# Performance work log

Measured on AMD Instinct MI355X. Metric: run time of the kernel, lower is better.

The kernel has to match this reference:

```python
import jax, jax.numpy as jnp
import numpy as np
from jax import lax

# --- config (matches init_kwargs) ---
D = 1024        # hidden_dim
H = 16          # num_heads
DH = D // H     # head dim
S = 5           # num_saccades
W = 128         # window_size
BK = 32         # block_size
TAU = 1.0       # gumbel temperature
DFF = 4 * D
EPS = 1e-5


def _ln(x, g, b):
    m = jnp.mean(x, axis=-1, keepdims=True)
    v = jnp.mean(jnp.square(x - m), axis=-1, keepdims=True)
    return (x - m) * lax.rsqrt(v + EPS) * g + b


def setup_inputs() -> dict:
    key = jax.random.key(0)
    ks = jax.random.split(key, 16)
    B, L = 4, 2048
    NB = L // BK
    sd = 0.02
    inp = {
        "hidden_states": jax.random.normal(ks[0], (B, L, D), jnp.float32),
        "gumbel_u": jax.random.uniform(ks[1], (S, B, NB), jnp.float32),
        "ln1_g": jnp.ones((D,), jnp.float32),
        "ln1_b": jnp.zeros((D,), jnp.float32),
        "ln2_g": jnp.ones((D,), jnp.float32),
        "ln2_b": jnp.zeros((D,), jnp.float32),
        "w_sal": jax.random.normal(ks[2], (D,), jnp.float32) * sd,
        "b_sal": jnp.zeros((), jnp.float32),
        "in_proj_w": jax.random.normal(ks[3], (3 * D, D), jnp.float32) * sd,
        "in_proj_b": jnp.zeros((3 * D,), jnp.float32),
        "out_proj_w": jax.random.normal(ks[4], (D, D), jnp.float32) * sd,
        "out_proj_b": jnp.zeros((D,), jnp.float32),
        "w_fc": jax.random.normal(ks[5], (D, DFF), jnp.float32) * sd,
        "b_fc": jnp.zeros((DFF,), jnp.float32),
        "w_proj": jax.random.normal(ks[6], (DFF, D), jnp.float32) * sd,
        "b_proj": jnp.zeros((D,), jnp.float32),
    }
    return inp


def reference(hidden_states, gumbel_u, ln1_g, ln1_b, ln2_g, ln2_b, w_sal, b_sal,
              in_proj_w, in_proj_b, out_proj_w, out_proj_b, w_fc, b_fc, w_proj, b_proj):
    x = hidden_states
    B, L, _ = x.shape
    NB = L // BK

    # ---- pre-norm ----
    h = _ln(x, ln1_g, ln1_b)

    # ---- peripheral map: mean-pool blocks, saliency logits ----
    blocks = h.reshape(B, NB, BK, D).mean(axis=2)          # (B, NB, D)
    logits = blocks @ w_sal + b_sal                        # (B, NB)

    # ---- gumbel-softmax hard block selection (straight-through) ----
    g = -jnp.log(-jnp.log(gumbel_u + 1e-9) + 1e-9)          # (S, B, NB)
    pert = (logits[None] + g) / TAU                         # (S, B, NB)
    p = jax.nn.softmax(pert, axis=-1)
    sel = jnp.argmax(pert, axis=-1)                         # (S, B) int
    w_soft = jnp.take_along_axis(p, sel[..., None], axis=-1)[..., 0]  # (S, B)
    scale = 1.0 + w_soft - lax.stop_gradient(w_soft)        # ST: fwd == 1

    # ---- gather fixation windows around selected block centers ----
    center = sel * BK + BK // 2
    start = jnp.clip(center - W // 2, 0, L - W)             # (S, B)
    idx = start[..., None] + jnp.arange(W)                  # (S, B, W)
    windows = h[jnp.arange(B)[None, :, None], idx, :]       # (S, B, W, D)
    windows = windows * scale[..., None, None]
    kv = windows.transpose(1, 0, 2, 3).reshape(B, S * W, D)  # (B, S*W, D)

    # ---- foveal MHA: queries = all tokens, keys/values = fixations ----
    wq, wk, wv = in_proj_w[:D], in_proj_w[D:2 * D], in_proj_w[2 * D:]
    bq, bk, bv = in_proj_b[:D], in_proj_b[D:2 * D], in_proj_b[2 * D:]
    q = (h @ wq.T + bq).reshape(B, L, H, DH)
    k = (kv @ wk.T + bk).reshape(B, S * W, H, DH)
    v = (kv @ wv.T + bv).reshape(B, S * W, H, DH)
    scores = jnp.einsum('blhd,bmhd->bhlm', q, k) / np.sqrt(DH).astype(np.float32)
    attn = jax.nn.softmax(scores, axis=-1)
    o = jnp.einsum('bhlm,bmhd->blhd', attn, v).reshape(B, L, D)
    o = o @ out_proj_w.T + out_proj_b

    x = x + o                                               # residual 1

    # ---- MLP (GPT-2: gelu-new) ----
    h2 = _ln(x, ln2_g, ln2_b)
    m = jax.nn.gelu(h2 @ w_fc + b_fc, approximate=True) @ w_proj + b_proj
    return x + m                                            # residual 2
```

## Files before the change

### kernel.cpp

```cpp
#include <hip/hip_runtime.h>

#define D_   1024
#define H_   16
#define DH_  64
#define S_   5
#define W_   128
#define BKB_ 32
#define DFF_ 4096
#define B_   4
#define L_   2048
#define NB_  64
#define SW_  (S_*W_)

typedef unsigned short u16;
typedef __attribute__((ext_vector_type(8))) short short8;
typedef __attribute__((ext_vector_type(4))) float floatx4;

__device__ __forceinline__ u16 f2bf(float f){
  unsigned int u = __float_as_uint(f);
  unsigned int r = 0x7fffu + ((u >> 16) & 1u);
  return (u16)((u + r) >> 16);
}

__device__ __forceinline__ void async_copy16(const u16* g, u16* lds){
  __builtin_amdgcn_global_load_lds(
      (const __attribute__((address_space(1))) void*)g,
      (__attribute__((address_space(3))) void*)lds, 16, 0, 0);
}

__device__ __forceinline__ float gelu_fast(float x){
  float u2 = 1.5957691216057308f * x * __builtin_fmaf(0.044715f, x*x, 1.0f);
  u2 = fminf(u2, 20.0f);
  float t = __expf(u2);
  return x * t * __builtin_amdgcn_rcpf(t + 1.0f);
}

__global__ void cast_f32_to_bf16(const float* __restrict__ in, u16* __restrict__ out, int n4){
  int i = blockIdx.x*256 + threadIdx.x;
  if (i < n4){
    float4 v = reinterpret_cast<const float4*>(in)[i];
    uint2 p;
    p.x = (unsigned)f2bf(v.x) | ((unsigned)f2bf(v.y) << 16);
    p.y = (unsigned)f2bf(v.z) | ((unsigned)f2bf(v.w) << 16);
    reinterpret_cast<uint2*>(out)[i] = p;
  }
}

__global__ void transpose_cast(const float* __restrict__ in, u16* __restrict__ out, int R, int C){
  __shared__ float t[32][33];
  int bx = blockIdx.x*32, by = blockIdx.y*32;
  int x = threadIdx.x & 31, y = threadIdx.x >> 5;
  #pragma unroll
  for (int i=0;i<4;i++)
    t[y + i*8][x] = in[(long long)(by + y + i*8)*C + bx + x];
  __syncthreads();
  #pragma unroll
  for (int i=0;i<4;i++)
    out[(long long)(bx + y + i*8)*R + by + x] = f2bf(t[x][y + i*8]);
}

template<bool ROWDOT>
__global__ __launch_bounds__(256) void ln_kernel(
    const float* __restrict__ x, const float* __restrict__ g, const float* __restrict__ b,
    const float* __restrict__ wsal, u16* __restrict__ out, float* __restrict__ logits)
{
  __shared__ float red[8];
  int row = blockIdx.x;
  int t = threadIdx.x;
  const float* xr = x + (long long)row*D_;
  float4 v = reinterpret_cast<const float4*>(xr)[t];
  float s  = v.x+v.y+v.z+v.w;
  float sq = v.x*v.x+v.y*v.y+v.z*v.z+v.w*v.w;
  #pragma unroll
  for (int m=32;m>=1;m>>=1){ s += __shfl_xor(s,m); sq += __shfl_xor(sq,m); }
  int wid = t>>6;
  if ((t&63)==0){ red[wid]=s; red[wid+4]=sq; }
  __syncthreads();
  s  = red[0]+red[1]+red[2]+red[3];
  sq = red[4]+red[5]+red[6]+red[7];
  float mean = s * (1.0f/D_);
  float var  = sq * (1.0f/D_) - mean*mean;
  float rstd = rsqrtf(fmaxf(var,0.0f) + 1e-5f);
  float4 gg = reinterpret_cast<const float4*>(g)[t];
  float4 bb = reinterpret_cast<const float4*>(b)[t];
  float h0 = (v.x-mean)*rstd*gg.x + bb.x;
  float h1 = (v.y-mean)*rstd*gg.y + bb.y;
  float h2 = (v.z-mean)*rstd*gg.z + bb.z;
  float h3 = (v.w-mean)*rstd*gg.w + bb.w;
  uint2 p;
  p.x = (unsigned)f2bf(h0) | ((unsigned)f2bf(h1) << 16);
  p.y = (unsigned)f2bf(h2) | ((unsigned)f2bf(h3) << 16);
  reinterpret_cast<uint2*>(out + (long long)row*D_)[t] = p;
  if (ROWDOT){
    float4 ww = reinterpret_cast<const float4*>(wsal)[t];
    float d = h0*ww.x + h1*ww.y + h2*ww.z + h3*ww.w;
    #pragma unroll
    for (int m=32;m>=1;m>>=1) d += __shfl_xor(d,m);
    __syncthreads();
    if ((t&63)==0) red[wid] = d;
    __syncthreads();
    if (t==0)
      atomicAdd(logits + (row>>5), (red[0]+red[1]+red[2]+red[3]) * (1.0f/BKB_));
  }
}

__global__ void select_kernel(const float* __restrict__ logits, const float* __restrict__ gum,
                              const float* __restrict__ bsal, int* __restrict__ start)
{
  int s = blockIdx.x >> 2, b = blockIdx.x & 3;
  int n = threadIdx.x;
  float u = gum[(s*B_ + b)*NB_ + n];
  float g = -logf(-logf(u + 1e-9f) + 1e-9f);
  float val = logits[b*NB_ + n] + bsal[0] + g;
  int idx = n;
  #pragma unroll
  for (int m=1;m<64;m<<=1){
    float ov = __shfl_xor(val, m);
    int   oi = __shfl_xor(idx, m);
    if (ov > val || (ov == val && oi < idx)) { val = ov; idx = oi; }
  }
  if (n==0){
    int c = idx*BKB_ + BKB_/2 - W_/2;
    c = c < 0 ? 0 : (c > (L_-W_) ? (L_-W_) : c);
    start[blockIdx.x] = c;
  }
}

__global__ void gather_kv(const u16* __restrict__ h, const int* __restrict__ start, u16* __restrict__ kv){
  int row = blockIdx.x;
  int b = row / SW_; int sw = row % SW_; int s = sw >> 7; int w = sw & 127;
  long long src = (long long)(b*L_ + start[s*B_ + b] + w)*D_;
  reinterpret_cast<uint2*>(kv + (long long)row*D_)[threadIdx.x] =
      reinterpret_cast<const uint2*>(h + src)[threadIdx.x];
}

__global__ __launch_bounds__(256) void transpose_v(const u16* __restrict__ v, u16* __restrict__ vT){
  __shared__ u16 t[64][72];
  const int bh = blockIdx.x;
  const int b = bh >> 4, h = bh & 15;
  const int mc = blockIdx.y * 64;
  const int r  = threadIdx.x >> 2;
  const int c0 = (threadIdx.x & 3) * 16;
  const u16* src = v + ((long long)(b*SW_ + mc + r)*D_ + h*DH_ + c0);
  *(uint4*)&t[r][c0]   = *(const uint4*)src;
  *(uint4*)&t[r][c0+8] = *(const uint4*)(src + 8);
  __syncthreads();
  u16 buf[16];
  #pragma unroll
  for (int j=0;j<16;j++) buf[j] = t[c0+j][r];
  uint4* dst = (uint4*)(vT + ((long long)(bh*DH_ + r)*SW_ + mc + c0));
  dst[0] = *(uint4*)&buf[0];
  dst[1] = *(uint4*)&buf[8];
}

template<int EPI>
__global__ __launch_bounds__(256) void gemm_bt(
    const u16* __restrict__ A, const u16* __restrict__ Bm,
    const float* __restrict__ bias, const float* __restrict__ res,
    void* __restrict__ Cout, int M, int N, int K)
{
  __shared__ u16 As[128*64];
  __shared__ u16 Bs[128*64];
  const int tid = threadIdx.x;
  const int wave = tid>>6, lane = tid&63;
  const int wr = wave>>1, wc = wave&1;
  const int quad = lane>>4, l16 = lane&15;
  const int rowA0 = blockIdx.x*128;
  const int colB0 = blockIdx.y*128;
  const int srow = wave*32 + (lane>>3);
  const int schunk = (lane&7) ^ ((lane>>3)&7);
  const u16* aP = A + (long long)(rowA0 + srow)*K + schunk*8;
  const u16* bP = Bm + (long long)(colB0 + srow)*K + schunk*8;
  u16* AsW = As + wave*2048;
  u16* BsW = Bs + wave*2048;
  const int sw16 = l16 & 7;
  floatx4 acc[4][4];
  #pragma unroll
  for (int i=0;i<4;i++)
    #pragma unroll
    for (int j=0;j<4;j++) acc[i][j] = (floatx4)0.0f;

  for (int kt=0; kt<K; kt+=64){
    #pragma unroll
    for (int t=0;t<4;t++){
      async_copy16(aP + (long long)t*8*K, AsW + t*512);
      async_copy16(bP + (long long)t*8*K, BsW + t*512);
    }
    aP += 64; bP += 64;
    __syncthreads();
    #pragma unroll
    for (int ks=0;ks<2;ks++){
      const int cA = ((ks*4 + quad) ^ sw16) * 8;
      short8 af[4], bfv[4];
      #pragma unroll
      for (int i=0;i<4;i++){
        af[i]  = *reinterpret_cast<const short8*>(As + (wr*64 + i*16 + l16)*64 + cA);
        bfv[i] = *reinterpret_cast<const short8*>(Bs + (wc*64 + i*16 + l16)*64 + cA);
      }
      #pragma unroll
      for (int i=0;i<4;i++)
        #pragma unroll
        for (int j=0;j<4;j++)
          acc[i][j] = __builtin_amdgcn_mfma_f32_16x16x32_bf16(af[i], bfv[j], acc[i][j], 0,0,0);
    }
    __syncthreads();
  }

  #pragma unroll
  for (int i=0;i<4;i++){
    #pragma unroll
    for (int j=0;j<4;j++){
      int row0 = rowA0 + wr*64 + i*16 + quad*4;
      int col  = colB0 + wc*64 + j*16 + l16;
      float bc = bias[col];
      #pragma unroll
      for (int r=0;r<4;r++){
        long long cidx = (long long)(row0+r)*N + col;
        float val = acc[i][j][r] + bc;
        if (EPI==0)      ((u16*)Cout)[cidx] = f2bf(val);
        else if (EPI==1) ((u16*)Cout)[cidx] = f2bf(gelu_fast(val));
        else             ((float*)Cout)[cidx] = val + res[cidx];
      }
    }
  }
}

__global__ __launch_bounds__(256) void attn_kernel(
    const u16* __restrict__ q, const u16* __restrict__ k, const u16* __restrict__ vT,
    u16* __restrict__ o)
{
  const int bh = blockIdx.x;
  const int b = bh >> 4, h = bh & 15;
  const int tid = threadIdx.x;
  const int wave = tid >> 6, lane = tid & 63;
  const int quad = lane >> 4, l16 = lane & 15;
  const int qrow0 = blockIdx.y*64 + wave*16;

  __shared__ u16 Ks[64*64];
  __shared__ u16 Vs[64*64];
  __shared__ u16 Ps[4][16*72];

  const u16* qp = q + ((long long)(b*L_ + qrow0 + l16)*D_ + h*DH_ + quad*8);
  short8 qf0 = *reinterpret_cast<const short8*>(qp);
  short8 qf1 = *reinterpret_cast<const short8*>(qp + 32);

  floatx4 Oacc[4];
  #pragma unroll
  for (int dt=0;dt<4;dt++) Oacc[dt] = (floatx4)0.0f;
  float lsum = 0.0f;

  const int srow = lane >> 3;
  const int scol = ((lane & 7) ^ srow) * 8;
  const int sw16 = l16 & 7;
  u16* PsW = Ps[wave];

  for (int mt=0; mt<SW_/64; ++mt){
    const int m0 = mt*64;
    __syncthreads();
    #pragma unroll
    for (int c=0;c<2;c++){
      int rk = wave*8 + c*32 + srow;
      async_copy16(k  + ((long long)(b*SW_ + m0 + rk)*D_ + h*DH_) + scol,
                   Ks + (wave*8 + c*32)*64);
      async_copy16(vT + ((long long)(bh*DH_ + rk)*SW_ + m0) + scol,
                   Vs + (wave*8 + c*32)*64);
    }
    __syncthreads();

    #pragma unroll
    for (int sub=0; sub<4; ++sub){
      short8 kf0 = *reinterpret_cast<const short8*>(Ks + (sub*16+l16)*64 + ((quad  ) ^ sw16)*8);
      short8 kf1 = *reinterpret_cast<const short8*>(Ks + (sub*16+l16)*64 + ((quad+4) ^ sw16)*8);
      floatx4 st = (floatx4)0.0f;
      st = __builtin_amdgcn_mfma_f32_16x16x32_bf16(kf0, qf0, st, 0,0,0);
      st = __builtin_amdgcn_mfma_f32_16x16x32_bf16(kf1, qf1, st, 0,0,0);
      float p0 = __expf(st[0]*0.125f);
      float p1 = __expf(st[1]*0.125f);
      float p2 = __expf(st[2]*0.125f);
      float p3 = __expf(st[3]*0.125f);
      lsum += (p0+p1) + (p2+p3);
      uint2 pk;
      pk.x = (unsigned)f2bf(p0) | ((unsigned)f2bf(p1) << 16);
      pk.y = (unsigned)f2bf(p2) | ((unsigned)f2bf(p3) << 16);
      *reinterpret_cast<uint2*>(PsW + l16*72 + sub*16 + quad*4) = pk;
    }

    short8 pf0 = *reinterpret_cast<const short8*>(PsW + l16*72 + quad*8);
    short8 pf1 = *reinterpret_cast<const short8*>(PsW + l16*72 + 32 + quad*8);

    #pragma unroll
    for (int dt=0; dt<4; ++dt){
      short8 vf0 = *reinterpret_cast<const short8*>(Vs + (dt*16+l16)*64 + ((quad  ) ^ sw16)*8);
      short8 vf1 = *reinterpret_cast<const short8*>(Vs + (dt*16+l16)*64 + ((quad+4) ^ sw16)*8);
      Oacc[dt] = __builtin_amdgcn_mfma_f32_16x16x32_bf16(pf0, vf0, Oacc[dt], 0,0,0);
      Oacc[dt] = __builtin_amdgcn_mfma_f32_16x16x32_bf16(pf1, vf1, Oacc[dt], 0,0,0);
    }
  }

  lsum += __shfl_xor(lsum, 16);
  lsum += __shfl_xor(lsum, 32);

  #pragma unroll
  for (int r=0;r<4;r++){
    float linv = 1.0f / __shfl(lsum, quad*4 + r);
    int qrow = qrow0 + quad*4 + r;
    #pragma unroll
    for (int dt=0;dt<4;dt++)
      o[((long long)(b*L_ + qrow))*D_ + h*DH_ + dt*16 + l16] = f2bf(Oacc[dt][r]*linv);
  }
}

extern "C" void kernel_launch(void* const* d_in, const int* in_sizes, int n_in,
                              void* d_out, int out_size, void* d_ws, size_t ws_size,
                              hipStream_t stream)
{
  const float* x     = (const float*)d_in[0];
  const float* gum   = (const float*)d_in[1];
  const float* ln1g  = (const float*)d_in[2];
  const float* ln1b  = (const float*)d_in[3];
  const float* ln2g  = (const float*)d_in[4];
  const float* ln2b  = (const float*)d_in[5];
  const float* wsal  = (const float*)d_in[6];
  const float* bsal  = (const float*)d_in[7];
  const float* inpw  = (const float*)d_in[8];
  const float* inpb  = (const float*)d_in[9];
  const float* outw  = (const float*)d_in[10];
  const float* outb  = (const float*)d_in[11];
  const float* wfc   = (const float*)d_in[12];
  const float* bfc   = (const float*)d_in[13];
  const float* wproj = (const float*)d_in[14];
  const float* bproj = (const float*)d_in[15];
  float* outp = (float*)d_out;
  char* ws = (char*)d_ws;

  const size_t BLD2 = (size_t)B_*L_*D_*2;
  size_t off = 0;
  auto alloc = [&](size_t n){ char* p = ws + off; off += (n + 1023) & ~(size_t)1023; return p; };
  u16*  WfcT   = (u16*)alloc((size_t)DFF_*D_*2);
  u16*  WprojT = (u16*)alloc((size_t)D_*DFF_*2);
  float* x2    = (float*)alloc((size_t)B_*L_*D_*4);
  float* logits= (float*)alloc(B_*NB_*4);
  int*  startb = (int*)alloc(S_*B_*4);
  char* regA = ws + off;
  size_t o1 = 0;
  auto alloc1 = [&](size_t n){ char* p = regA + o1; o1 += (n + 1023) & ~(size_t)1023; return p; };
  u16* h_buf = (u16*)alloc1(BLD2);
  u16* Wqkv  = (u16*)alloc1((size_t)3*D_*D_*2);
  u16* Wout  = (u16*)alloc1((size_t)D_*D_*2);
  u16* qb    = (u16*)alloc1(BLD2);
  u16* kvb   = (u16*)alloc1((size_t)B_*SW_*D_*2);
  u16* kb    = (u16*)alloc1((size_t)B_*SW_*D_*2);
  u16* vb    = (u16*)alloc1((size_t)B_*SW_*D_*2);
  u16* vTb   = (u16*)alloc1((size_t)B_*SW_*D_*2);
  u16* ob    = (u16*)alloc1(BLD2);
  u16* h2b = (u16*)regA;
  u16* act = (u16*)(regA + ((BLD2 + 1023) & ~(size_t)1023));

  hipMemsetAsync(logits, 0, B_*NB_*4, stream);

  cast_f32_to_bf16<<<3*D_*D_/1024, 256, 0, stream>>>(inpw, Wqkv, 3*D_*D_/4);
  cast_f32_to_bf16<<<D_*D_/1024,   256, 0, stream>>>(outw, Wout, D_*D_/4);
  transpose_cast<<<dim3(DFF_/32, D_/32), 256, 0, stream>>>(wfc,   WfcT,   D_,   DFF_);
  transpose_cast<<<dim3(D_/32, DFF_/32), 256, 0, stream>>>(wproj, WprojT, DFF_, D_);

  ln_kernel<true><<<B_*L_, 256, 0, stream>>>(x, ln1g, ln1b, wsal, h_buf, logits);
  select_kernel<<<S_*B_, 64, 0, stream>>>(logits, gum, bsal, startb);
  gather_kv<<<B_*SW_, 256, 0, stream>>>(h_buf, startb, kvb);

  gemm_bt<0><<<dim3(B_*L_/128,  D_/128), 256, 0, stream>>>(h_buf, Wqkv,            inpb,        nullptr, qb, B_*L_,  D_, D_);
  gemm_bt<0><<<dim3(B_*SW_/128, D_/128), 256, 0, stream>>>(kvb,   Wqkv +   D_*D_,  inpb +   D_, nullptr, kb, B_*SW_, D_, D_);
  gemm_bt<0><<<dim3(B_*SW_/128, D_/128), 256, 0, stream>>>(kvb,   Wqkv + 2*D_*D_,  inpb + 2*D_, nullptr, vb, B_*SW_, D_, D_);

  transpose_v<<<dim3(B_*H_, SW_/64), 256, 0, stream>>>(vb, vTb);

  attn_kernel<<<dim3(B_*H_, L_/64), 256, 0, stream>>>(qb, kb, vTb, ob);

  gemm_bt<2><<<dim3(B_*L_/128, D_/128), 256, 0, stream>>>(ob, Wout, outb, x, x2, B_*L_, D_, D_);

  ln_kernel<false><<<B_*L_, 256, 0, stream>>>(x2, ln2g, ln2b, nullptr, h2b, nullptr);

  gemm_bt<1><<<dim3(B_*L_/128, DFF_/128), 256, 0, stream>>>(h2b, WfcT,   bfc,   nullptr, act,  B_*L_, DFF_, D_);
  gemm_bt<2><<<dim3(B_*L_/128, D_/128),   256, 0, stream>>>(act, WprojT, bproj, x2,      outp, B_*L_, D_,   DFF_);
}
```

Measured before the change: 505.3 us.

## Double-buffer GEMM LDS tiles and fuse K/V projection with transposed V epilogue

The GEMM main loop changes from a single 64-wide K tile with two barriers per step to double-buffered 32-wide K tiles. The next tile's async copy is issued before the current tile's MFMAs, so global loads overlap compute and one barrier per step is dropped. The separate K and V projection GEMMs become one GEMM over 2*D output columns. Its new epilogue writes V directly in transposed per-head layout, which removes the transpose_v kernel and the intermediate V buffer. In exchange, the K-tile is smaller and each iteration does fewer MFMAs, and the transposed V stores are narrow strided writes.

```diff
diff --git a/kernel.cpp b/kernel.cpp
--- a/kernel.cpp
+++ b/kernel.cpp
@@ -134,76 +134,64 @@
       reinterpret_cast<const uint2*>(h + src)[threadIdx.x];
 }
 
-__global__ __launch_bounds__(256) void transpose_v(const u16* __restrict__ v, u16* __restrict__ vT){
-  __shared__ u16 t[64][72];
-  const int bh = blockIdx.x;
-  const int b = bh >> 4, h = bh & 15;
-  const int mc = blockIdx.y * 64;
-  const int r  = threadIdx.x >> 2;
-  const int c0 = (threadIdx.x & 3) * 16;
-  const u16* src = v + ((long long)(b*SW_ + mc + r)*D_ + h*DH_ + c0);
-  *(uint4*)&t[r][c0]   = *(const uint4*)src;
-  *(uint4*)&t[r][c0+8] = *(const uint4*)(src + 8);
-  __syncthreads();
-  u16 buf[16];
-  #pragma unroll
-  for (int j=0;j<16;j++) buf[j] = t[c0+j][r];
-  uint4* dst = (uint4*)(vT + ((long long)(bh*DH_ + r)*SW_ + mc + c0));
-  dst[0] = *(uint4*)&buf[0];
-  dst[1] = *(uint4*)&buf[8];
-}
-
 template<int EPI>
 __global__ __launch_bounds__(256) void gemm_bt(
     const u16* __restrict__ A, const u16* __restrict__ Bm,
     const float* __restrict__ bias, const float* __restrict__ res,
-    void* __restrict__ Cout, int M, int N, int K)
-{
-  __shared__ u16 As[128*64];
-  __shared__ u16 Bs[128*64];
+    void* __restrict__ Cout, void* __restrict__ Cout2, int M, int N, int K)
+{
+  __shared__ u16 As[2][128*32];
+  __shared__ u16 Bs[2][128*32];
   const int tid = threadIdx.x;
   const int wave = tid>>6, lane = tid&63;
   const int wr = wave>>1, wc = wave&1;
   const int quad = lane>>4, l16 = lane&15;
   const int rowA0 = blockIdx.x*128;
   const int colB0 = blockIdx.y*128;
-  const int srow = wave*32 + (lane>>3);
-  const int schunk = (lane&7) ^ ((lane>>3)&7);
-  const u16* aP = A + (long long)(rowA0 + srow)*K + schunk*8;
-  const u16* bP = Bm + (long long)(colB0 + srow)*K + schunk*8;
-  u16* AsW = As + wave*2048;
-  u16* BsW = Bs + wave*2048;
-  const int sw16 = l16 & 7;
+  const int r0  = tid>>2;
+  const int cst = (tid&3) ^ ((tid>>2)&3);
+  const u16* aP0 = A  + (long long)(rowA0 + r0     )*K + cst*8;
+  const u16* aP1 = A  + (long long)(rowA0 + 64 + r0)*K + cst*8;
+  const u16* bP0 = Bm + (long long)(colB0 + r0     )*K + cst*8;
+  const u16* bP1 = Bm + (long long)(colB0 + 64 + r0)*K + cst*8;
+  u16* ldsA = &As[0][0] + wave*512;
+  u16* ldsB = &Bs[0][0] + wave*512;
+  const int swq = l16 & 3;
   floatx4 acc[4][4];
   #pragma unroll
   for (int i=0;i<4;i++)
     #pragma unroll
     for (int j=0;j<4;j++) acc[i][j] = (floatx4)0.0f;
 
-  for (int kt=0; kt<K; kt+=64){
-    #pragma unroll
-    for (int t=0;t<4;t++){
-      async_copy16(aP + (long long)t*8*K, AsW + t*512);
-      async_copy16(bP + (long long)t*8*K, BsW + t*512);
-    }
-    aP += 64; bP += 64;
-    __syncthreads();
-    #pragma unroll
-    for (int ks=0;ks<2;ks++){
-      const int cA = ((ks*4 + quad) ^ sw16) * 8;
-      short8 af[4], bfv[4];
+  const int T = K >> 5;
+  async_copy16(aP0, ldsA);
+  async_copy16(aP1, ldsA + 2048);
+  async_copy16(bP0, ldsB);
+  async_copy16(bP1, ldsB + 2048);
+
+  for (int t=0; t<T; ++t){
+    __syncthreads();
+    if (t+1 < T){
+      const int nb = (t+1)&1, ko = (t+1)<<5;
+      async_copy16(aP0 + ko, ldsA + nb*4096);
+      async_copy16(aP1 + ko, ldsA + nb*4096 + 2048);
+      async_copy16(bP0 + ko, ldsB + nb*4096);
+      async_copy16(bP1 + ko, ldsB + nb*4096 + 2048);
+    }
+    const u16* Ab = &As[t&1][0];
+    const u16* Bb = &Bs[t&1][0];
+    short8 af[4], bfv[4];
+    #pragma unroll
+    for (int i=0;i<4;i++){
+      const int co = ((quad ^ swq))*8;
+      af[i]  = *reinterpret_cast<const short8*>(Ab + (wr*64 + i*16 + l16)*32 + co);
+      bfv[i] = *reinterpret_cast<const short8*>(Bb + (wc*64 + i*16 + l16)*32 + co);
+    }
+    #pragma unroll
+    for (int i=0;i<4;i++)
       #pragma unroll
-      for (int i=0;i<4;i++){
-        af[i]  = *reinterpret_cast<const short8*>(As + (wr*64 + i*16 + l16)*64 + cA);
-        bfv[i] = *reinterpret_cast<const short8*>(Bs + (wc*64 + i*16 + l16)*64 + cA);
-      }
-      #pragma unroll
-      for (int i=0;i<4;i++)
-        #pragma unroll
-        for (int j=0;j<4;j++)
-          acc[i][j] = __builtin_amdgcn_mfma_f32_16x16x32_bf16(af[i], bfv[j], acc[i][j], 0,0,0);
-    }
-    __syncthreads();
+      for (int j=0;j<4;j++)
+        acc[i][j] = __builtin_amdgcn_mfma_f32_16x16x32_bf16(af[i], bfv[j], acc[i][j], 0,0,0);
   }
 
   #pragma unroll
@@ -213,13 +201,29 @@
       int row0 = rowA0 + wr*64 + i*16 + quad*4;
       int col  = colB0 + wc*64 + j*16 + l16;
       float bc = bias[col];
-      #pragma unroll
-      for (int r=0;r<4;r++){
-        long long cidx = (long long)(row0+r)*N + col;
-        float val = acc[i][j][r] + bc;
-        if (EPI==0)      ((u16*)Cout)[cidx] = f2bf(val);
-        else if (EPI==1) ((u16*)Cout)[cidx] = f2bf(gelu_fast(val));
-        else             ((float*)Cout)[cidx] = val + res[cidx];
+      if (EPI==3){
+        if (col < 1024){
+          #pragma unroll
+          for (int r=0;r<4;r++)
+            ((u16*)Cout)[(long long)(row0+r)*1024 + col] = f2bf(acc[i][j][r] + bc);
+        } else {
+          int vcol = col - 1024;
+          int h = vcol >> 6, dh = vcol & 63;
+          int b = row0 / SW_, mm = row0 % SW_;
+          uint2 pk;
+          pk.x = (unsigned)f2bf(acc[i][j][0]+bc) | ((unsigned)f2bf(acc[i][j][1]+bc) << 16);
+          pk.y = (unsigned)f2bf(acc[i][j][2]+bc) | ((unsigned)f2bf(acc[i][j][3]+bc) << 16);
+          *reinterpret_cast<uint2*>((u16*)Cout2 + ((long long)((b*H_ + h)*DH_ + dh))*SW_ + mm) = pk;
+        }
+      } else {
+        #pragma unroll
+        for (int r=0;r<4;r++){
+          long long cidx = (long long)(row0+r)*N + col;
+          float val = acc[i][j][r] + bc;
+          if (EPI==0)      ((u16*)Cout)[cidx] = f2bf(val);
+          else if (EPI==1) ((u16*)Cout)[cidx] = f2bf(gelu_fast(val));
+          else             ((float*)Cout)[cidx] = val + res[cidx];
+        }
       }
     }
   }
@@ -350,7 +354,6 @@
   u16* qb    = (u16*)alloc1(BLD2);
   u16* kvb   = (u16*)alloc1((size_t)B_*SW_*D_*2);
   u16* kb    = (u16*)alloc1((size_t)B_*SW_*D_*2);
-  u16* vb    = (u16*)alloc1((size_t)B_*SW_*D_*2);
   u16* vTb   = (u16*)alloc1((size_t)B_*SW_*D_*2);
   u16* ob    = (u16*)alloc1(BLD2);
   u16* h2b = (u16*)regA;
@@ -367,18 +370,15 @@
   select_kernel<<<S_*B_, 64, 0, stream>>>(logits, gum, bsal, startb);
   gather_kv<<<B_*SW_, 256, 0, stream>>>(h_buf, startb, kvb);
 
-  gemm_bt<0><<<dim3(B_*L_/128,  D_/128), 256, 0, stream>>>(h_buf, Wqkv,            inpb,        nullptr, qb, B_*L_,  D_, D_);
-  gemm_bt<0><<<dim3(B_*SW_/128, D_/128), 256, 0, stream>>>(kvb,   Wqkv +   D_*D_,  inpb +   D_, nullptr, kb, B_*SW_, D_, D_);
-  gemm_bt<0><<<dim3(B_*SW_/128, D_/128), 256, 0, stream>>>(kvb,   Wqkv + 2*D_*D_,  inpb + 2*D_, nullptr, vb, B_*SW_, D_, D_);
-
-  transpose_v<<<dim3(B_*H_, SW_/64), 256, 0, stream>>>(vb, vTb);
+  gemm_bt<0><<<dim3(B_*L_/128,  D_/128), 256, 0, stream>>>(h_buf, Wqkv, inpb, nullptr, qb, nullptr, B_*L_, D_, D_);
+  gemm_bt<3><<<dim3(B_*SW_/128, 2*D_/128), 256, 0, stream>>>(kvb, Wqkv + D_*D_, inpb + D_, nullptr, kb, vTb, B_*SW_, 2*D_, D_);
 
   attn_kernel<<<dim3(B_*H_, L_/64), 256, 0, stream>>>(qb, kb, vTb, ob);
 
-  gemm_bt<2><<<dim3(B_*L_/128, D_/128), 256, 0, stream>>>(ob, Wout, outb, x, x2, B_*L_, D_, D_);
+  gemm_bt<2><<<dim3(B_*L_/128, D_/128), 256, 0, stream>>>(ob, Wout, outb, x, x2, nullptr, B_*L_, D_, D_);
 
   ln_kernel<false><<<B_*L_, 256, 0, stream>>>(x2, ln2g, ln2b, nullptr, h2b, nullptr);
 
-  gemm_bt<1><<<dim3(B_*L_/128, DFF_/128), 256, 0, stream>>>(h2b, WfcT,   bfc,   nullptr, act,  B_*L_, DFF_, D_);
-  gemm_bt<2><<<dim3(B_*L_/128, D_/128),   256, 0, stream>>>(act, WprojT, bproj, x2,      outp, B_*L_, D_,   DFF_);
-}
+  gemm_bt<1><<<dim3(B_*L_/128, DFF_/128), 256, 0, stream>>>(h2b, WfcT,   bfc,   nullptr, act,  nullptr, B_*L_, DFF_, D_);
+  gemm_bt<2><<<dim3(B_*L_/128, D_/128),   256, 0, stream>>>(act, WprojT, bproj, x2,      outp, nullptr, B_*L_, D_,   DFF_);
+}
```

Result: no change. 497.3 us (-1.6%).
